# Kernel optimization log

Hardware: AMD Instinct MI355X
Metric: run time of the kernel (lower is better)

Reference implementation:

```python
import jax, jax.numpy as jnp
import numpy as np

B, V, H = 16384, 1024, 256


def setup_inputs() -> dict:
    key = jax.random.key(0)
    k1, k2 = jax.random.split(key)
    # binary spin configurations in {0,1}
    batch = jax.random.bernoulli(k1, 0.5, (B, V)).astype(jnp.float32)
    # small weights + negative hidden bias keep exp(log p*) finite in fp32
    weights_amp = jax.random.normal(k2, (H, V), dtype=jnp.float32) * (0.05 / np.sqrt(V))
    visible_bias_amp = jnp.zeros((V,), dtype=jnp.float32)
    hidden_bias_amp = -5.0 * jnp.ones((H,), dtype=jnp.float32)
    return {
        'batch': batch,
        'weights_amp': weights_amp,
        'visible_bias_amp': visible_bias_amp,
        'hidden_bias_amp': hidden_bias_amp,
        'k': 8,
    }


def _gibbs_sampling_amp(v0, W, vb, hb, k, key):
    """k steps of block Gibbs sampling, vectorized over the whole batch [B,V]."""
    keys = jax.random.split(key, 2 * k).reshape(k, 2)

    def step(v, ks):
        ph = jax.nn.sigmoid(v @ W.T + hb)                      # [B,H]
        h = (jax.random.uniform(ks[0], ph.shape) < ph).astype(v.dtype)
        pv = jax.nn.sigmoid(h @ W + vb)                        # [B,V]
        v = (jax.random.uniform(ks[1], pv.shape) < pv).astype(v.dtype)
        return v, None

    vk, _ = jax.lax.scan(step, v0, keys)
    return vk


def reference(batch, weights_amp, visible_bias_amp, hidden_bias_amp, k):
    W, vb, hb = weights_amp, visible_bias_amp, hidden_bias_amp
    nbatch = batch.shape[0]
    key = jax.random.key(42)

    vk = _gibbs_sampling_amp(batch, W, vb, hb, k, key)          # [B,V]

    ph0 = jax.nn.sigmoid(batch @ W.T + hb)                      # [B,H] positive-phase hidden probs
    pre_k = vk @ W.T + hb                                       # [B,H]
    phk = jax.nn.sigmoid(pre_k)                                 # [B,H] negative-phase hidden probs

    # unnormalized_probability_amp(vk) = exp(vk.vb + sum_j softplus((W vk + hb)_j))
    log_p = vk @ vb + jax.nn.softplus(pre_k).sum(axis=-1)       # [B]
    inv_norm = jnp.exp(-log_p) / nbatch                         # 1 / (len(batch) * p*(vk))

    # g_W = sum_b [outer(phk_b, vk_b) - outer(ph0_b, v0_b)] / norm_b
    g_w = (jnp.einsum('b,bh,bv->hv', inv_norm, phk, vk)
           - jnp.einsum('b,bh,bv->hv', inv_norm, ph0, batch))   # [H,V]
    g_vb = jnp.einsum('b,bv->v', inv_norm, vk - batch)          # [V]
    g_hb = jnp.einsum('b,bh->h', inv_norm, phk - ph0)           # [H]

    return jnp.concatenate([g_w.ravel(), g_vb, g_hb])
```

## Files before the change

kernel.cpp:

```cpp
#include <hip/hip_runtime.h>
#include <stdint.h>

#define B_DIM 16384
#define V_DIM 1024
#define H_DIM 256
#define K_STEPS 8
#define HALF_B 8192

typedef short bf16x8 __attribute__((ext_vector_type(8)));
typedef float f32x4 __attribute__((ext_vector_type(4)));

__host__ __device__ inline uint32_t rotl32(uint32_t v, int r) {
#if defined(__HIP_DEVICE_COMPILE__)
    return __builtin_amdgcn_alignbit(v, v, (uint32_t)(32 - r));
#else
    return (v << r) | (v >> (32 - r));
#endif
}

__host__ __device__ inline void threefry2x32(uint32_t k0, uint32_t k1,
                                             uint32_t x0, uint32_t x1,
                                             uint32_t* o0, uint32_t* o1) {
    uint32_t k2 = k0 ^ k1 ^ 0x1BD11BDAu;
    x0 += k0; x1 += k1;
#define TF_RND(r) { x0 += x1; x1 = rotl32(x1, (r)); x1 ^= x0; }
    TF_RND(13) TF_RND(15) TF_RND(26) TF_RND(6)
    x0 += k1; x1 += k2 + 1u;
    TF_RND(17) TF_RND(29) TF_RND(16) TF_RND(24)
    x0 += k2; x1 += k0 + 2u;
    TF_RND(13) TF_RND(15) TF_RND(26) TF_RND(6)
    x0 += k0; x1 += k1 + 3u;
    TF_RND(17) TF_RND(29) TF_RND(16) TF_RND(24)
    x0 += k1; x1 += k2 + 4u;
    TF_RND(13) TF_RND(15) TF_RND(26) TF_RND(6)
    x0 += k2; x1 += k0 + 5u;
#undef TF_RND
    *o0 = x0; *o1 = x1;
}

__device__ inline float tf_uniform(uint32_t key0, uint32_t key1, uint32_t e) {
    uint32_t o0, o1;
    threefry2x32(key0, key1, 0u, e, &o0, &o1);
    uint32_t bits = o0 ^ o1;
    return __uint_as_float((bits >> 9) | 0x3f800000u) - 1.0f;
}

__device__ inline uint16_t bf16_rn(float f) {
    uint32_t u = __float_as_uint(f);
    uint32_t r = u + 0x7FFFu + ((u >> 16) & 1u);
    return (uint16_t)(r >> 16);
}
__device__ inline float bf16_to_f32(uint16_t h) {
    return __uint_as_float(((uint32_t)h) << 16);
}

__device__ inline void gload_lds16(const void* g, void* l) {
    __builtin_amdgcn_global_load_lds((const __attribute__((address_space(1))) uint32_t*)g,
                                     (__attribute__((address_space(3))) uint32_t*)l, 16, 0, 0);
}


__global__ void pack_w_kernel(const float* __restrict__ W,
                              ushort* __restrict__ whp, ushort* __restrict__ wlp) {
    int uid = blockIdx.x * 256 + threadIdx.x;
    int l = uid & 63, s = (uid >> 6) & 1, kc = (uid >> 7) & 15, R = uid >> 11;
    int row = R * 16 + (l & 15);
    int col = kc * 64 + s * 32 + (l >> 4) * 8;
    const float* src = W + (size_t)row * V_DIM + col;
    ushort* dh = whp + (size_t)uid * 8;
    ushort* dl = wlp + (size_t)uid * 8;
#pragma unroll
    for (int e = 0; e < 8; ++e) {
        float w = src[e];
        ushort hi = bf16_rn(w);
        dh[e] = hi;
        dl[e] = bf16_rn(w - bf16_to_f32(hi));
    }
}

__global__ void pack_batch_kernel(const float* __restrict__ batch,
                                  ushort* __restrict__ bp) {
    int uid = blockIdx.x * 256 + threadIdx.x;
    int l = uid & 63, s = (uid >> 6) & 1, kc = (uid >> 7) & 15, R = uid >> 11;
    int row = R * 16 + (l & 15);
    int col = kc * 64 + s * 32 + (l >> 4) * 8;
    const float* src = batch + (size_t)row * V_DIM + col;
    ushort* d = bp + (size_t)uid * 8;
#pragma unroll
    for (int e = 0; e < 8; ++e) d[e] = bf16_rn(src[e]);
}

template <int MODE>
__device__ __forceinline__ void gemm_block_p(
    const int m0, const int n0,
    const ushort* __restrict__ Ap, const ushort* __restrict__ Bhp,
    const ushort* __restrict__ Blp, const float* __restrict__ bias,
    ushort* __restrict__ out, ushort* __restrict__ out2,
    const uint32_t key0, const uint32_t key1) {
    const int lane = threadIdx.x & 63;
    const int w = threadIdx.x >> 6;
    const int wm = (w & 1) * 32;
    const int wn = (w >> 1) * 32;
    const int q = lane >> 4;
    const int l15 = lane & 15;

    const ushort* apA = Ap + (size_t)((m0 >> 4) + (wm >> 4)) * 16384 + lane * 8;
    const ushort* apBh = Bhp + (size_t)((n0 >> 4) + (wn >> 4)) * 16384 + lane * 8;
    const ushort* apBl = Blp + (size_t)((n0 >> 4) + (wn >> 4)) * 16384 + lane * 8;

    f32x4 acc[2][2] = {};

#pragma unroll 2
    for (int kc = 0; kc < 16; ++kc) {
#pragma unroll
        for (int s = 0; s < 2; ++s) {
            const int go = kc * 1024 + s * 512;
            bf16x8 af[2], bh[2], bl[2];
#pragma unroll
            for (int i = 0; i < 2; ++i)
                af[i] = *(const bf16x8*)(apA + go + i * 16384);
#pragma unroll
            for (int j = 0; j < 2; ++j) {
                bh[j] = *(const bf16x8*)(apBh + go + j * 16384);
                bl[j] = *(const bf16x8*)(apBl + go + j * 16384);
            }
#pragma unroll
            for (int i = 0; i < 2; ++i)
#pragma unroll
                for (int j = 0; j < 2; ++j) {
                    acc[i][j] = __builtin_amdgcn_mfma_f32_16x16x32_bf16(af[i], bh[j], acc[i][j], 0, 0, 0);
                    acc[i][j] = __builtin_amdgcn_mfma_f32_16x16x32_bf16(af[i], bl[j], acc[i][j], 0, 0, 0);
                }
        }
    }

    const int orow = q * 4;
#pragma unroll
    for (int i = 0; i < 2; ++i) {
#pragma unroll
        for (int j = 0; j < 2; ++j) {
            int col = n0 + wn + j * 16 + l15;
            float bv = bias[col];
#pragma unroll
            for (int r = 0; r < 4; ++r) {
                int row = m0 + wm + i * 16 + orow + r;
                float val = acc[i][j][r] + bv;
                if (MODE == 0) {
                    float E = expf(-val);
                    uint32_t e = (uint32_t)row * (uint32_t)H_DIM + (uint32_t)col;
                    float u = tf_uniform(key0, key1, e);
                    out[(size_t)row * H_DIM + col] = (fmaf(u, E, u) < 1.0f) ? (ushort)0x3F80 : (ushort)0;
                } else if (MODE == 3) {
                    float E = expf(-val);
                    float sg = 1.0f / (1.0f + E);
                    uint32_t e = (uint32_t)row * (uint32_t)H_DIM + (uint32_t)col;
                    float u = tf_uniform(key0, key1, e);
                    out[(size_t)row * H_DIM + col] = (fmaf(u, E, u) < 1.0f) ? (ushort)0x3F80 : (ushort)0;
                    out2[(size_t)row * H_DIM + col] = bf16_rn(sg);
                } else {
                    float sg = 1.0f / (1.0f + expf(-val));
                    out[(size_t)row * H_DIM + col] = bf16_rn(sg);
                }
            }
        }
    }
}

__device__ __forceinline__ void vsample_block(
    const ushort* __restrict__ h, const float* __restrict__ W,
    const float* __restrict__ vb, ushort* __restrict__ vpack,
    ushort* __restrict__ vrow, int write_row,
    uint32_t key0, uint32_t key1, int row_base) {
    const int lane = threadIdx.x & 63;
    const int wid = threadIdx.x >> 6;

    float vbr[16];
#pragma unroll
    for (int t = 0; t < 16; ++t) vbr[t] = vb[lane + 64 * t];

    const int rb2 = row_base + wid * 2;
#pragma unroll
    for (int rr = 0; rr < 2; ++rr) {
        const int b = rb2 + rr;
        ushort4 hv = ((const ushort4*)(h + (size_t)b * H_DIM))[lane];
        unsigned long long masks[4];
        masks[0] = __ballot(hv.x != 0);
        masks[1] = __ballot(hv.y != 0);
        masks[2] = __ballot(hv.z != 0);
        masks[3] = __ballot(hv.w != 0);

        float acc[16];
#pragma unroll
        for (int t = 0; t < 16; ++t) acc[t] = 0.0f;

#pragma unroll
        for (int s = 0; s < 4; ++s) {
            unsigned long long m = masks[s];
            while (m) {
                int l = __ffsll(m) - 1;
                m &= m - 1;
                int j = l * 4 + s;
                const float* wrow = W + (size_t)j * V_DIM + lane;
#pragma unroll
                for (int t = 0; t < 16; ++t) acc[t] += wrow[64 * t];
            }
        }

        const uint32_t ebase = (uint32_t)b * (uint32_t)V_DIM + (uint32_t)lane;
        ushort* vp = vpack + (size_t)(b >> 4) * 16384 + (b & 15) * 8 +
                     ((lane >> 5) & 1) * 512 + ((lane >> 3) & 3) * 128 + (lane & 7);
        ushort* orow = vrow + (size_t)b * V_DIM + lane;
#pragma unroll
        for (int t = 0; t < 16; ++t) {
            float pre = acc[t] + vbr[t];
            float E = expf(-pre);
            float u = tf_uniform(key0, key1, ebase + 64u * (uint32_t)t);
            ushort val = (fmaf(u, E, u) < 1.0f) ? (ushort)0x3F80 : (ushort)0;
            vp[t * 1024] = val;
            if (write_row) orow[64 * t] = val;
        }
    }
}

template <int MODE>
__global__ __launch_bounds__(256, 6) void gemm_only(
    const ushort* __restrict__ Ap, const ushort* __restrict__ Bhp,
    const ushort* __restrict__ Blp, const float* __restrict__ bias,
    ushort* __restrict__ out, ushort* __restrict__ out2,
    uint32_t key0, uint32_t key1, int mbase) {
    gemm_block_p<MODE>(mbase + blockIdx.x * 64, blockIdx.y * 64, Ap, Bhp, Blp,
                       bias, out, out2, key0, key1);
}

template <int MODE>
__global__ __launch_bounds__(256, 6) void hybrid_step(
    const ushort* __restrict__ Ap, const ushort* __restrict__ Whp,
    const ushort* __restrict__ Wlp, const float* __restrict__ hb,
    ushort* __restrict__ hout, ushort* __restrict__ out2,
    uint32_t gk0, uint32_t gk1, int gemm_mbase,
    const ushort* __restrict__ hprev, const float* __restrict__ Wf,
    const float* __restrict__ vb, ushort* __restrict__ vpack,
    ushort* __restrict__ vrow, int write_row,
    uint32_t vk0, uint32_t vk1, int vs_base) {
    const int bid = blockIdx.x;
    const int g3 = bid / 3;
    const int r3 = bid - g3 * 3;
    if (r3 < 2) {
        const int vs = g3 * 2 + r3;
        vsample_block(hprev, Wf, vb, vpack, vrow, write_row, vk0, vk1,
                      vs_base + vs * 8);
    } else {
        const int g = g3;
        const int gx = g & 127;
        const int gy = g >> 7;
        gemm_block_p<MODE>(gemm_mbase + gx * 64, gy * 64, Ap, Whp, Wlp, hb,
                           hout, out2, gk0, gk1);
    }
}

__global__ __launch_bounds__(256, 4) void mfma_gemm_acc(
    const ushort* __restrict__ A, const ushort* __restrict__ Bt,
    float* __restrict__ out, int N, int K, int k_slice) {
    __shared__ __align__(16) ushort As[64 * 64];
    __shared__ __align__(16) ushort Bs[64 * 64];

    const int tid = threadIdx.x;
    const int lane = tid & 63;
    const int w = tid >> 6;
    const int m0 = blockIdx.x * 64;
    const int n0 = blockIdx.y * 64;
    const int kbase = blockIdx.z * k_slice;

    const int wm = (w & 1) * 32;
    const int wn = (w >> 1) * 32;
    const int q = lane >> 4;
    const int l15 = lane & 15;

    const ushort* asrc[2];
    const ushort* bsrc[2];
#pragma unroll
    for (int i = 0; i < 2; ++i) {
        const int j = w * 2 + i;
        const int row = j * 8 + (lane >> 3);
        const int sl = (lane & 7) ^ (row & 7);
        const size_t off = (size_t)row * K + (sl >> 2) * 32 + (sl & 3) * 8;
        asrc[i] = A + (size_t)m0 * K + off;
        bsrc[i] = Bt + (size_t)n0 * K + off;
    }

    f32x4 acc[2][2] = {};

    for (int kt = 0; kt < k_slice; kt += 64) {
        const int k0 = kbase + kt;
#pragma unroll
        for (int i = 0; i < 2; ++i) {
            gload_lds16(asrc[i] + k0, &As[(w * 2 + i) * 512]);
            gload_lds16(bsrc[i] + k0, &Bs[(w * 2 + i) * 512]);
        }
        __syncthreads();
#pragma unroll
        for (int s = 0; s < 2; ++s) {
            bf16x8 af[2], bf[2];
#pragma unroll
            for (int i = 0; i < 2; ++i) {
                const int ra = wm + i * 16 + l15;
                const int rb = wn + i * 16 + l15;
                af[i] = *(const bf16x8*)((const char*)As + ra * 128 +
                                         (((s * 4 + q) ^ (ra & 7)) * 16));
                bf[i] = *(const bf16x8*)((const char*)Bs + rb * 128 +
                                         (((s * 4 + q) ^ (rb & 7)) * 16));
            }
#pragma unroll
            for (int i = 0; i < 2; ++i)
#pragma unroll
                for (int j = 0; j < 2; ++j)
                    acc[i][j] = __builtin_amdgcn_mfma_f32_16x16x32_bf16(af[i], bf[j], acc[i][j], 0, 0, 0);
        }
        __syncthreads();
    }

    const int orow = q * 4;
#pragma unroll
    for (int i = 0; i < 2; ++i)
#pragma unroll
        for (int j = 0; j < 2; ++j) {
            int col = n0 + wn + j * 16 + l15;
#pragma unroll
            for (int r = 0; r < 4; ++r) {
                int row = m0 + wm + i * 16 + orow + r;
                atomicAdd(&out[(size_t)row * N + col], acc[i][j][r]);
            }
        }
}

__global__ __launch_bounds__(256) void lognorm_kernel(
    const ushort* __restrict__ phk, const ushort* __restrict__ vk,
    const float* __restrict__ vb, float* __restrict__ inv) {
    int b = blockIdx.x;
    int tid = threadIdx.x;
    float p = bf16_to_f32(phk[(size_t)b * H_DIM + tid]);
    float s = -log1pf(-p);
    for (int j = tid; j < V_DIM; j += 256)
        s += bf16_to_f32(vk[(size_t)b * V_DIM + j]) * vb[j];
    for (int off = 32; off > 0; off >>= 1) s += __shfl_down(s, off, 64);
    __shared__ float wsum[4];
    int lane = tid & 63, wid = tid >> 6;
    if (lane == 0) wsum[wid] = s;
    __syncthreads();
    if (tid == 0) {
        float t = wsum[0] + wsum[1] + wsum[2] + wsum[3];
        inv[b] = expf(-t) * (1.0f / 16384.0f);
    }
}

__global__ void build_At(const ushort* __restrict__ P, const float* __restrict__ inv,
                         float sgn, ushort* __restrict__ At) {
    __shared__ float T[64][65];
    int c = threadIdx.x & 63;
    int rb = threadIdx.x >> 6;
    int b0 = blockIdx.x * 64;
    int h0 = blockIdx.y * 64;
    for (int r = rb; r < 64; r += 4) {
        int b = b0 + r;
        T[c][r] = sgn * inv[b] * bf16_to_f32(P[(size_t)b * H_DIM + h0 + c]);
    }
    __syncthreads();
    for (int r = rb; r < 64; r += 4)
        At[(size_t)(h0 + r) * B_DIM + b0 + c] = bf16_rn(T[r][c]);
}

__global__ void build_Bt(const ushort* __restrict__ Sb, const float* __restrict__ Sf,
                         int use_f32, ushort* __restrict__ Bt) {
    __shared__ ushort T[64][65];
    int c = threadIdx.x & 63;
    int rb = threadIdx.x >> 6;
    int b0 = blockIdx.x * 64;
    int v0 = blockIdx.y * 64;
    for (int r = rb; r < 64; r += 4) {
        int b = b0 + r;
        T[c][r] = use_f32 ? bf16_rn(Sf[(size_t)b * V_DIM + v0 + c])
                          : Sb[(size_t)b * V_DIM + v0 + c];
    }
    __syncthreads();
    for (int r = rb; r < 64; r += 4)
        Bt[(size_t)(v0 + r) * B_DIM + b0 + c] = T[r][c];
}

__global__ void gvb_kernel(const ushort* __restrict__ vk, const float* __restrict__ batchf,
                           const float* __restrict__ inv, float* __restrict__ gvb) {
    int col = blockIdx.x * 256 + threadIdx.x;
    int b0 = blockIdx.y * 512;
    float acc = 0.0f;
    for (int r = 0; r < 512; ++r) {
        int b = b0 + r;
        acc += inv[b] * (bf16_to_f32(vk[(size_t)b * V_DIM + col]) -
                         batchf[(size_t)b * V_DIM + col]);
    }
    atomicAdd(&gvb[col], acc);
}

__global__ void ghb_kernel(const ushort* __restrict__ phk, const ushort* __restrict__ ph0,
                           const float* __restrict__ inv, float* __restrict__ ghb) {
    int col = threadIdx.x;
    int b0 = blockIdx.x * 256;
    float acc = 0.0f;
    for (int r = 0; r < 256; ++r) {
        int b = b0 + r;
        acc += inv[b] * (bf16_to_f32(phk[(size_t)b * H_DIM + col]) -
                         bf16_to_f32(ph0[(size_t)b * H_DIM + col]));
    }
    atomicAdd(&ghb[col], acc);
}

extern "C" void kernel_launch(void* const* d_in, const int* in_sizes, int n_in,
                              void* d_out, int out_size, void* d_ws, size_t ws_size,
                              hipStream_t stream) {
    const float* batch = (const float*)d_in[0];
    const float* W = (const float*)d_in[1];
    const float* vb = (const float*)d_in[2];
    const float* hb = (const float*)d_in[3];

    char* base = (char*)d_ws;
    ushort* w_hi_p = (ushort*)(base + 0);
    ushort* w_lo_p = (ushort*)(base + 524288);
    float*  inv    = (float*)(base + 1048576);
    ushort* v_pack = (ushort*)(base + 2097152);
    ushort* Bt     = v_pack;
    ushort* v_row  = (ushort*)(base + 35651584);
    ushort* batch_p = v_row;
    ushort* h_cur  = (ushort*)(base + 69206016);
    ushort* At     = h_cur;
    ushort* ph0b   = (ushort*)(base + 77594624);
    ushort* phkb   = (ushort*)(base + 85983232);

    float* gw  = (float*)d_out;
    float* gvb = gw + (size_t)H_DIM * V_DIM;
    float* ghb = gvb + V_DIM;

    hipMemsetAsync(d_out, 0, (size_t)out_size * sizeof(float), stream);

    uint32_t sk0[16], sk1[16];
    for (int n = 0; n < 16; ++n) threefry2x32(0u, 42u, 0u, (uint32_t)n, &sk0[n], &sk1[n]);

    pack_w_kernel<<<dim3(128), dim3(256), 0, stream>>>(W, w_hi_p, w_lo_p);
    pack_batch_kernel<<<dim3(8192), dim3(256), 0, stream>>>(batch, batch_p);

    const int NB_VS = HALF_B / 8;
    const int NB_G  = (HALF_B / 64) * 4;
    const dim3 HYB(NB_VS + NB_G);

    gemm_only<3><<<dim3(128, 4), dim3(256), 0, stream>>>(
        batch_p, w_hi_p, w_lo_p, hb, h_cur, ph0b, sk0[0], sk1[0], 0);

    for (int s = 0; s < K_STEPS; ++s) {
        const int wr = (s == K_STEPS - 1) ? 1 : 0;
        if (s == 0) {
            hybrid_step<3><<<HYB, dim3(256), 0, stream>>>(
                batch_p, w_hi_p, w_lo_p, hb, h_cur, ph0b, sk0[0], sk1[0], HALF_B,
                h_cur, W, vb, v_pack, v_row, wr, sk0[1], sk1[1], 0);
        } else {
            hybrid_step<0><<<HYB, dim3(256), 0, stream>>>(
                v_pack, w_hi_p, w_lo_p, hb, h_cur, nullptr, sk0[2 * s], sk1[2 * s], HALF_B,
                h_cur, W, vb, v_pack, v_row, wr, sk0[2 * s + 1], sk1[2 * s + 1], 0);
        }
        if (s < K_STEPS - 1) {
            hybrid_step<0><<<HYB, dim3(256), 0, stream>>>(
                v_pack, w_hi_p, w_lo_p, hb, h_cur, nullptr, sk0[2 * s + 2], sk1[2 * s + 2], 0,
                h_cur, W, vb, v_pack, v_row, wr, sk0[2 * s + 1], sk1[2 * s + 1], HALF_B);
        } else {
            hybrid_step<1><<<HYB, dim3(256), 0, stream>>>(
                v_pack, w_hi_p, w_lo_p, hb, phkb, nullptr, 0u, 0u, 0,
                h_cur, W, vb, v_pack, v_row, wr, sk0[2 * s + 1], sk1[2 * s + 1], HALF_B);
        }
    }
    gemm_only<1><<<dim3(128, 4), dim3(256), 0, stream>>>(
        v_pack, w_hi_p, w_lo_p, hb, phkb, nullptr, 0u, 0u, HALF_B);

    lognorm_kernel<<<dim3(B_DIM), dim3(256), 0, stream>>>(phkb, v_row, vb, inv);
    ghb_kernel<<<dim3(B_DIM / 256), dim3(256), 0, stream>>>(phkb, ph0b, inv, ghb);
    gvb_kernel<<<dim3(V_DIM / 256, B_DIM / 512), dim3(256), 0, stream>>>(v_row, batch, inv, gvb);

    build_At<<<dim3(B_DIM / 64, H_DIM / 64), dim3(256), 0, stream>>>(phkb, inv, 1.0f, At);
    build_Bt<<<dim3(B_DIM / 64, V_DIM / 64), dim3(256), 0, stream>>>(v_row, nullptr, 0, Bt);
    mfma_gemm_acc<<<dim3(H_DIM / 64, V_DIM / 64, 16), dim3(256), 0, stream>>>(
        At, Bt, gw, V_DIM, B_DIM, 1024);
    build_At<<<dim3(B_DIM / 64, H_DIM / 64), dim3(256), 0, stream>>>(ph0b, inv, -1.0f, At);
    build_Bt<<<dim3(B_DIM / 64, V_DIM / 64), dim3(256), 0, stream>>>(nullptr, batch, 1, Bt);
    mfma_gemm_acc<<<dim3(H_DIM / 64, V_DIM / 64, 16), dim3(256), 0, stream>>>(
        At, Bt, gw, V_DIM, B_DIM, 1024);
}
```

Before: 862.1 us.

## Mix vsample and GEMM work per wave inside each hybrid block

Restructures the hybrid Gibbs-step kernel so that each 192-thread block holds two visible-sampling waves and one GEMM wave, replacing the earlier scheme of whole 256-thread blocks dedicated to one role. The GEMM and sampling routines become per-wave units with explicit row/column offsets. The aim is to co-schedule the MFMA-bound and the latency/ALU-bound work on the same CU more evenly and to reduce tail imbalance between block types. GEMM waves in a block no longer share a 64x64 tile, so locality across waves within a block may drop.

```diff
diff --git a/kernel.cpp b/kernel.cpp
--- a/kernel.cpp
+++ b/kernel.cpp
@@ -91,22 +91,19 @@
 }
 
 template <int MODE>
-__device__ __forceinline__ void gemm_block_p(
-    const int m0, const int n0,
+__device__ __forceinline__ void gemm_wave_unit(
+    const int m0w, const int n0w,
     const ushort* __restrict__ Ap, const ushort* __restrict__ Bhp,
     const ushort* __restrict__ Blp, const float* __restrict__ bias,
     ushort* __restrict__ out, ushort* __restrict__ out2,
     const uint32_t key0, const uint32_t key1) {
     const int lane = threadIdx.x & 63;
-    const int w = threadIdx.x >> 6;
-    const int wm = (w & 1) * 32;
-    const int wn = (w >> 1) * 32;
     const int q = lane >> 4;
     const int l15 = lane & 15;
 
-    const ushort* apA = Ap + (size_t)((m0 >> 4) + (wm >> 4)) * 16384 + lane * 8;
-    const ushort* apBh = Bhp + (size_t)((n0 >> 4) + (wn >> 4)) * 16384 + lane * 8;
-    const ushort* apBl = Blp + (size_t)((n0 >> 4) + (wn >> 4)) * 16384 + lane * 8;
+    const ushort* apA = Ap + (size_t)(m0w >> 4) * 16384 + lane * 8;
+    const ushort* apBh = Bhp + (size_t)(n0w >> 4) * 16384 + lane * 8;
+    const ushort* apBl = Blp + (size_t)(n0w >> 4) * 16384 + lane * 8;
 
     f32x4 acc[2][2] = {};
 
@@ -139,11 +136,11 @@
     for (int i = 0; i < 2; ++i) {
 #pragma unroll
         for (int j = 0; j < 2; ++j) {
-            int col = n0 + wn + j * 16 + l15;
+            int col = n0w + j * 16 + l15;
             float bv = bias[col];
 #pragma unroll
             for (int r = 0; r < 4; ++r) {
-                int row = m0 + wm + i * 16 + orow + r;
+                int row = m0w + i * 16 + orow + r;
                 float val = acc[i][j][r] + bv;
                 if (MODE == 0) {
                     float E = expf(-val);
@@ -166,22 +163,20 @@
     }
 }
 
-__device__ __forceinline__ void vsample_block(
+__device__ __forceinline__ void vsample_wave_unit(
     const ushort* __restrict__ h, const float* __restrict__ W,
     const float* __restrict__ vb, ushort* __restrict__ vpack,
     ushort* __restrict__ vrow, int write_row,
-    uint32_t key0, uint32_t key1, int row_base) {
+    uint32_t key0, uint32_t key1, int row2) {
     const int lane = threadIdx.x & 63;
-    const int wid = threadIdx.x >> 6;
 
     float vbr[16];
 #pragma unroll
     for (int t = 0; t < 16; ++t) vbr[t] = vb[lane + 64 * t];
 
-    const int rb2 = row_base + wid * 2;
 #pragma unroll
     for (int rr = 0; rr < 2; ++rr) {
-        const int b = rb2 + rr;
+        const int b = row2 + rr;
         ushort4 hv = ((const ushort4*)(h + (size_t)b * H_DIM))[lane];
         unsigned long long masks[4];
         masks[0] = __ballot(hv.x != 0);
@@ -228,12 +223,14 @@
     const ushort* __restrict__ Blp, const float* __restrict__ bias,
     ushort* __restrict__ out, ushort* __restrict__ out2,
     uint32_t key0, uint32_t key1, int mbase) {
-    gemm_block_p<MODE>(mbase + blockIdx.x * 64, blockIdx.y * 64, Ap, Bhp, Blp,
-                       bias, out, out2, key0, key1);
+    const int w = threadIdx.x >> 6;
+    const int m0w = mbase + blockIdx.x * 64 + (w & 1) * 32;
+    const int n0w = blockIdx.y * 64 + (w >> 1) * 32;
+    gemm_wave_unit<MODE>(m0w, n0w, Ap, Bhp, Blp, bias, out, out2, key0, key1);
 }
 
 template <int MODE>
-__global__ __launch_bounds__(256, 6) void hybrid_step(
+__global__ __launch_bounds__(192, 6) void hybrid_step(
     const ushort* __restrict__ Ap, const ushort* __restrict__ Whp,
     const ushort* __restrict__ Wlp, const float* __restrict__ hb,
     ushort* __restrict__ hout, ushort* __restrict__ out2,
@@ -243,18 +240,16 @@
     ushort* __restrict__ vrow, int write_row,
     uint32_t vk0, uint32_t vk1, int vs_base) {
     const int bid = blockIdx.x;
-    const int g3 = bid / 3;
-    const int r3 = bid - g3 * 3;
-    if (r3 < 2) {
-        const int vs = g3 * 2 + r3;
-        vsample_block(hprev, Wf, vb, vpack, vrow, write_row, vk0, vk1,
-                      vs_base + vs * 8);
+    const int w = threadIdx.x >> 6;
+    if (w < 2) {
+        const int u = bid * 2 + w;
+        vsample_wave_unit(hprev, Wf, vb, vpack, vrow, write_row, vk0, vk1,
+                          vs_base + u * 2);
     } else {
-        const int g = g3;
-        const int gx = g & 127;
-        const int gy = g >> 7;
-        gemm_block_p<MODE>(gemm_mbase + gx * 64, gy * 64, Ap, Whp, Wlp, hb,
-                           hout, out2, gk0, gk1);
+        const int gm = bid & 255;
+        const int gn = bid >> 8;
+        gemm_wave_unit<MODE>(gemm_mbase + gm * 32, gn * 32, Ap, Whp, Wlp, hb,
+                             hout, out2, gk0, gk1);
     }
 }
 
@@ -445,9 +440,8 @@
     pack_w_kernel<<<dim3(128), dim3(256), 0, stream>>>(W, w_hi_p, w_lo_p);
     pack_batch_kernel<<<dim3(8192), dim3(256), 0, stream>>>(batch, batch_p);
 
-    const int NB_VS = HALF_B / 8;
-    const int NB_G  = (HALF_B / 64) * 4;
-    const dim3 HYB(NB_VS + NB_G);
+    const dim3 HYB(2048);
+    const dim3 HYBT(192);
 
     gemm_only<3><<<dim3(128, 4), dim3(256), 0, stream>>>(
         batch_p, w_hi_p, w_lo_p, hb, h_cur, ph0b, sk0[0], sk1[0], 0);
@@ -455,20 +449,20 @@
     for (int s = 0; s < K_STEPS; ++s) {
         const int wr = (s == K_STEPS - 1) ? 1 : 0;
         if (s == 0) {
-            hybrid_step<3><<<HYB, dim3(256), 0, stream>>>(
+            hybrid_step<3><<<HYB, HYBT, 0, stream>>>(
                 batch_p, w_hi_p, w_lo_p, hb, h_cur, ph0b, sk0[0], sk1[0], HALF_B,
                 h_cur, W, vb, v_pack, v_row, wr, sk0[1], sk1[1], 0);
         } else {
-            hybrid_step<0><<<HYB, dim3(256), 0, stream>>>(
+            hybrid_step<0><<<HYB, HYBT, 0, stream>>>(
                 v_pack, w_hi_p, w_lo_p, hb, h_cur, nullptr, sk0[2 * s], sk1[2 * s], HALF_B,
                 h_cur, W, vb, v_pack, v_row, wr, sk0[2 * s + 1], sk1[2 * s + 1], 0);
         }
         if (s < K_STEPS - 1) {
-            hybrid_step<0><<<HYB, dim3(256), 0, stream>>>(
+            hybrid_step<0><<<HYB, HYBT, 0, stream>>>(
                 v_pack, w_hi_p, w_lo_p, hb, h_cur, nullptr, sk0[2 * s + 2], sk1[2 * s + 2], 0,
                 h_cur, W, vb, v_pack, v_row, wr, sk0[2 * s + 1], sk1[2 * s + 1], HALF_B);
         } else {
-            hybrid_step<1><<<HYB, dim3(256), 0, stream>>>(
+            hybrid_step<1><<<HYB, HYBT, 0, stream>>>(
                 v_pack, w_hi_p, w_lo_p, hb, phkb, nullptr, 0u, 0u, 0,
                 h_cur, W, vb, v_pack, v_row, wr, sk0[2 * s + 1], sk1[2 * s + 1], HALF_B);
         }
```

New measurement: 883.7 us. 1.03x slower.
